# Kernel optimization log

Measured on AMD Instinct MI355X. Metric: run time of the kernel, lower is better.

Reference implementation:

```python
import jax, jax.numpy as jnp
import numpy as np

V, E, L, D, B, S = 50000, 512, 1024, 10, 1024, 50
N_NODES = L - 1  # internal Huffman nodes (balanced tree from uniform label counts)
LN_EPS = 1e-5
N_HIDDEN = 10


def _build_tree():
    # balanced binary tree in heap order: node at depth t for leaf l is (2^t - 1) + (l >> (D - t))
    l = np.arange(L)[:, None]
    t = np.arange(D)[None, :]
    bits = ((l >> (D - 1 - t)) & 1).astype(np.int32)          # [L, D] path direction bits
    paths = ((2 ** t - 1) + (l >> (D - t))).astype(np.int32)  # [L, D] internal node ids
    return paths, bits


def setup_inputs() -> dict:
    key = jax.random.key(0)
    k1, k2, k3, k4, k5, k6 = jax.random.split(key, 6)
    paths, bits = _build_tree()
    return {
        "input_ids": jax.random.randint(k1, (B, S), 0, V),
        "emb_table": jax.random.normal(k2, (V, E), dtype=jnp.float32) * 0.02,
        "W_h": jax.random.normal(k3, (E, E), dtype=jnp.float32) * (1.0 / np.sqrt(E)),
        "b_h": jax.random.normal(k4, (E,), dtype=jnp.float32) * 0.01,
        "theta_W": jax.random.normal(k5, (N_NODES, E, 2), dtype=jnp.float32) * (1.0 / np.sqrt(E)),
        "theta_b": jax.random.normal(k6, (N_NODES, 2), dtype=jnp.float32) * 0.01,
        "paths": jnp.asarray(paths),
        "bits": jnp.asarray(bits),
    }


def reference(input_ids, emb_table, W_h, b_h, theta_W, theta_b, paths, bits):
    # embedding + mean pool over sequence
    x = jnp.take(emb_table, input_ids, axis=0).mean(axis=1)  # [B, E]
    # LayerNorm with default (non-learned) affine, created fresh in torch forward
    mu = x.mean(axis=-1, keepdims=True)
    var = x.var(axis=-1, keepdims=True)
    x = (x - mu) * jax.lax.rsqrt(var + LN_EPS)
    # repeated hidden linear (same weights, hidden_num times)
    for _ in range(N_HIDDEN):
        x = x @ W_h + b_h
    # hierarchical softmax: batched 2-way logits at every internal node
    logits = jnp.einsum('be,ned->bnd', x, theta_W) + theta_b  # [B, N, 2]
    probs = jax.nn.softmax(logits, axis=-1)                   # [B, N, 2]
    # gather each class's path probs and multiply along the path
    p = probs[:, paths, bits]                                  # [B, L, D]
    return jnp.prod(p, axis=-1)                                # [B, L]
```

## Files before the change

### kernel.cpp

```cpp
#include <hip/hip_runtime.h>
#include <math.h>

#define B_  1024
#define S_  50
#define E_  512
#define L_  1024
#define D_  10
#define NN  1023
#define LN_EPS 1e-5f
#define CBLK 72

typedef short short8 __attribute__((ext_vector_type(8)));
typedef float f32x4  __attribute__((ext_vector_type(4)));

union PackU { unsigned int u[4]; short8 s; };

__device__ inline void split8(const float r[8], short8& hi, short8& lo) {
    PackU H, L;
#pragma unroll
    for (int q = 0; q < 4; ++q) {
        const unsigned int u0 = __float_as_uint(r[2*q+0]);
        const unsigned int u1 = __float_as_uint(r[2*q+1]);
        H.u[q] = (u0 >> 16) | (u1 & 0xFFFF0000u);
        const float h0 = __uint_as_float(u0 & 0xFFFF0000u);
        const float h1 = __uint_as_float(u1 & 0xFFFF0000u);
        const float l0 = r[2*q+0] - h0;
        const float l1 = r[2*q+1] - h1;
        unsigned int p;
        asm("v_cvt_pk_bf16_f32 %0, %1, %2" : "=v"(p) : "v"(l0), "v"(l1));
        L.u[q] = p;
    }
    hi = H.s; lo = L.s;
}

struct FragBuf { float4 a[2][2]; float4 b[2][2]; };

__device__ inline void loadbuf(FragBuf& f,
                               const float* pa0, const float* pa1,
                               const float* pb0, const float* pb1, int off) {
    f.a[0][0] = *reinterpret_cast<const float4*>(pa0 + off);
    f.a[0][1] = *reinterpret_cast<const float4*>(pa0 + off + 4);
    f.a[1][0] = *reinterpret_cast<const float4*>(pa1 + off);
    f.a[1][1] = *reinterpret_cast<const float4*>(pa1 + off + 4);
    f.b[0][0] = *reinterpret_cast<const float4*>(pb0 + off);
    f.b[0][1] = *reinterpret_cast<const float4*>(pb0 + off + 4);
    f.b[1][0] = *reinterpret_cast<const float4*>(pb1 + off);
    f.b[1][1] = *reinterpret_cast<const float4*>(pb1 + off + 4);
}

template<int TERMS>
__device__ inline void compbuf(const FragBuf& f, f32x4 acc[2][2]) {
    short8 ah[2], al[2], bh[2], bl[2];
#pragma unroll
    for (int i = 0; i < 2; ++i) {
        const float ra[8] = {f.a[i][0].x, f.a[i][0].y, f.a[i][0].z, f.a[i][0].w,
                             f.a[i][1].x, f.a[i][1].y, f.a[i][1].z, f.a[i][1].w};
        split8(ra, ah[i], al[i]);
        const float rb[8] = {f.b[i][0].x, f.b[i][0].y, f.b[i][0].z, f.b[i][0].w,
                             f.b[i][1].x, f.b[i][1].y, f.b[i][1].z, f.b[i][1].w};
        split8(rb, bh[i], bl[i]);
    }
#pragma unroll
    for (int i = 0; i < 2; ++i)
#pragma unroll
        for (int j = 0; j < 2; ++j) {
            acc[i][j] = __builtin_amdgcn_mfma_f32_16x16x32_bf16(ah[i], bh[j], acc[i][j], 0, 0, 0);
            acc[i][j] = __builtin_amdgcn_mfma_f32_16x16x32_bf16(ah[i], bl[j], acc[i][j], 0, 0, 0);
            acc[i][j] = __builtin_amdgcn_mfma_f32_16x16x32_bf16(al[i], bh[j], acc[i][j], 0, 0, 0);
            if (TERMS == 4)
                acc[i][j] = __builtin_amdgcn_mfma_f32_16x16x32_bf16(al[i], bl[j], acc[i][j], 0, 0, 0);
        }
}

template<int TERMS>
__device__ inline void gemm_k512(const float* pa0, const float* pa1,
                                 const float* pb0, const float* pb1,
                                 f32x4 acc[2][2]) {
    FragBuf f0, f1;
    loadbuf(f0, pa0, pa1, pb0, pb1, 0);
#pragma unroll 1
    for (int kt = 0; kt < 16; kt += 2) {
        loadbuf(f1, pa0, pa1, pb0, pb1, (kt + 1) * 32);
        compbuf<TERMS>(f0, acc);
        if (kt + 2 < 16) loadbuf(f0, pa0, pa1, pb0, pb1, (kt + 2) * 32);
        compbuf<TERMS>(f1, acc);
    }
}

__device__ inline void do_embed_row(const int* __restrict__ ids,
                                    const float* __restrict__ emb,
                                    float* __restrict__ x, int b) {
    const int t = threadIdx.x;
    float a0 = 0.f, a1 = 0.f;
    const int* idr = ids + b * S_;
#pragma unroll 5
    for (int s = 0; s < S_; ++s) {
        const float2 v = *reinterpret_cast<const float2*>(emb + (long)idr[s] * E_ + 2 * t);
        a0 += v.x;
        a1 += v.y;
    }
    a0 *= (1.f / S_);
    a1 *= (1.f / S_);

    __shared__ float red[256];
    red[t] = a0 + a1;
    __syncthreads();
    for (int off = 128; off > 0; off >>= 1) {
        if (t < off) red[t] += red[t + off];
        __syncthreads();
    }
    const float mean = red[0] * (1.f / E_);
    __syncthreads();
    const float d0 = a0 - mean, d1 = a1 - mean;
    red[t] = d0 * d0 + d1 * d1;
    __syncthreads();
    for (int off = 128; off > 0; off >>= 1) {
        if (t < off) red[t] += red[t + off];
        __syncthreads();
    }
    const float var = red[0] * (1.f / E_);
    const float inv = 1.f / sqrtf(var + LN_EPS);
    float2 o; o.x = d0 * inv; o.y = d1 * inv;
    *reinterpret_cast<float2*>(x + b * E_ + 2 * t) = o;
}

__device__ inline void do_dpack(const float* __restrict__ thW,
                                float* __restrict__ Dm, int part) {
    const int total = NN * 256;
    const int nth = 64 * 256;
    for (int p = part * 256 + (int)threadIdx.x; p < total; p += nth) {
        const int n = p >> 8;
        const int kp = p & 255;
        const float4 v = *reinterpret_cast<const float4*>(thW + (long)n * 1024 + kp * 4);
        float2 d; d.x = v.y - v.x; d.y = v.w - v.z;
        *reinterpret_cast<float2*>(Dm + (long)n * E_ + kp * 2) = d;
    }
}

__device__ inline void do_compose0(const float* __restrict__ Wh, const float* __restrict__ bh,
                                   float* __restrict__ Q0, float* __restrict__ T0, int bid) {
    const int tid  = threadIdx.x;
    const int wid  = tid >> 6;
    const int lane = tid & 63;
    const int r_lo = lane & 15;
    const int kg   = lane >> 4;
    const int row_base = (bid >> 3) * 64 + (wid >> 1) * 32;
    const int col_base = (bid & 7) * 64 + (wid & 1) * 32;
    f32x4 acc[2][2] = {};
#pragma unroll 2
    for (int kt = 0; kt < E_; kt += 32) {
        const int ks = kt + kg * 8;
        short8 ah[2], al[2], bhf[2], blf[2];
#pragma unroll
        for (int i = 0; i < 2; ++i) {
            const int row = row_base + i * 16 + r_lo;
            const float* ap = (row < E_) ? (Wh + (long)row * E_ + ks) : (bh + ks);
            const float4 v0 = *reinterpret_cast<const float4*>(ap);
            const float4 v1 = *reinterpret_cast<const float4*>(ap + 4);
            const float rr[8] = {v0.x, v0.y, v0.z, v0.w, v1.x, v1.y, v1.z, v1.w};
            split8(rr, ah[i], al[i]);
        }
#pragma unroll
        for (int j = 0; j < 2; ++j) {
            const int c = col_base + j * 16 + r_lo;
            float rr[8];
#pragma unroll
            for (int q = 0; q < 8; ++q) rr[q] = Wh[(long)(ks + q) * E_ + c];
            split8(rr, bhf[j], blf[j]);
        }
#pragma unroll
        for (int i = 0; i < 2; ++i)
#pragma unroll
            for (int j = 0; j < 2; ++j) {
                acc[i][j] = __builtin_amdgcn_mfma_f32_16x16x32_bf16(ah[i], bhf[j], acc[i][j], 0, 0, 0);
                acc[i][j] = __builtin_amdgcn_mfma_f32_16x16x32_bf16(ah[i], blf[j], acc[i][j], 0, 0, 0);
                acc[i][j] = __builtin_amdgcn_mfma_f32_16x16x32_bf16(al[i], bhf[j], acc[i][j], 0, 0, 0);
                acc[i][j] = __builtin_amdgcn_mfma_f32_16x16x32_bf16(al[i], blf[j], acc[i][j], 0, 0, 0);
            }
    }
#pragma unroll
    for (int j = 0; j < 2; ++j) {
        const int col = col_base + j * 16 + r_lo;
        const float bb = bh[col];
#pragma unroll
        for (int i = 0; i < 2; ++i) {
            const int row0 = row_base + i * 16 + kg * 4;
            float4 tv;
#pragma unroll
            for (int r2 = 0; r2 < 4; ++r2) {
                const int row = row0 + r2;
                float v = acc[i][j][r2];
                if (row == E_) v += bb;
                if (row <= E_) Q0[(long)row * E_ + col] = v;
                ((float*)&tv)[r2] = v;
            }
            if (row0 + 3 < E_) {
                *reinterpret_cast<float4*>(T0 + (long)col * E_ + row0) = tv;
            }
        }
    }
}

__device__ inline void do_compose(const float* __restrict__ A,
                                  const float* __restrict__ Bt,
                                  const float* __restrict__ Bbias,
                                  float* __restrict__ C, float* __restrict__ Ct,
                                  int bid) {
    const int tid  = threadIdx.x;
    const int wid  = tid >> 6;
    const int lane = tid & 63;
    const int r_lo = lane & 15;
    const int kg   = lane >> 4;
    const int row_base = (bid >> 3) * 64 + (wid >> 1) * 32;
    const int col_base = (bid & 7) * 64 + (wid & 1) * 32;

    int ra0 = row_base + r_lo;        if (ra0 > E_) ra0 = E_;
    int ra1 = row_base + 16 + r_lo;   if (ra1 > E_) ra1 = E_;
    const float* pa0 = A + (long)ra0 * E_ + kg * 8;
    const float* pa1 = A + (long)ra1 * E_ + kg * 8;
    const float* pb0 = Bt + (long)(col_base + r_lo) * E_ + kg * 8;
    const float* pb1 = Bt + (long)(col_base + 16 + r_lo) * E_ + kg * 8;

    f32x4 acc[2][2] = {};
    gemm_k512<4>(pa0, pa1, pb0, pb1, acc);

#pragma unroll
    for (int j = 0; j < 2; ++j) {
        const int col = col_base + j * 16 + r_lo;
        const float bb = Bbias[col];
#pragma unroll
        for (int i = 0; i < 2; ++i) {
            const int row0 = row_base + i * 16 + kg * 4;
            float4 tv;
#pragma unroll
            for (int r2 = 0; r2 < 4; ++r2) {
                const int row = row0 + r2;
                float v = acc[i][j][r2];
                if (row == E_) v += bb;
                if (row <= E_) C[(long)row * E_ + col] = v;
                ((float*)&tv)[r2] = v;
            }
            if (row0 + 3 < E_) {
                *reinterpret_cast<float4*>(Ct + (long)col * E_ + row0) = tv;
            }
        }
    }
}

__device__ inline void do_apply(const float* __restrict__ X,
                                const float* __restrict__ Mt,
                                const float* __restrict__ bias,
                                float* __restrict__ Y,
                                int tr, int tc) {
    const int tid  = threadIdx.x;
    const int wid  = tid >> 6;
    const int lane = tid & 63;
    const int r_lo = lane & 15;
    const int kg   = lane >> 4;
    const int row_base = tr * 64 + (wid >> 1) * 32;
    const int col_base = tc * 64 + (wid & 1) * 32;

    const float* pa0 = X + (long)(row_base + r_lo) * E_ + kg * 8;
    const float* pa1 = X + (long)(row_base + 16 + r_lo) * E_ + kg * 8;
    const float* pb0 = Mt + (long)(col_base + r_lo) * E_ + kg * 8;
    const float* pb1 = Mt + (long)(col_base + 16 + r_lo) * E_ + kg * 8;

    f32x4 acc[2][2] = {};
    gemm_k512<3>(pa0, pa1, pb0, pb1, acc);

#pragma unroll
    for (int j = 0; j < 2; ++j) {
        const int col = col_base + j * 16 + r_lo;
        const float bb = bias[col];
#pragma unroll
        for (int i = 0; i < 2; ++i) {
#pragma unroll
            for (int r2 = 0; r2 < 4; ++r2) {
                const int row = row_base + i * 16 + kg * 4 + r2;
                Y[(long)row * E_ + col] = acc[i][j][r2] + bb;
            }
        }
    }
}

__global__ __launch_bounds__(256) void k_fused0(const float* __restrict__ Wh,
                                                const float* __restrict__ bh,
                                                float* __restrict__ Q0, float* __restrict__ T0,
                                                const int* __restrict__ ids,
                                                const float* __restrict__ emb,
                                                float* __restrict__ xa,
                                                const float* __restrict__ thW,
                                                float* __restrict__ Dm) {
    const int bid = blockIdx.x;
    if (bid < CBLK)            do_compose0(Wh, bh, Q0, T0, bid);
    else if (bid < CBLK + 512) do_embed_row(ids, emb, xa, bid - CBLK);
    else                       do_dpack(thW, Dm, bid - CBLK - 512);
}

__global__ __launch_bounds__(256) void k_fused1(const float* __restrict__ Q0,
                                                const float* __restrict__ T0,
                                                float* __restrict__ Q1, float* __restrict__ T1,
                                                const int* __restrict__ ids,
                                                const float* __restrict__ emb,
                                                float* __restrict__ xa) {
    const int bid = blockIdx.x;
    if (bid < CBLK) do_compose(Q0, T0, Q0 + (long)E_ * E_, Q1, T1, bid);
    else            do_embed_row(ids, emb, xa, 512 + (bid - CBLK));
}

__global__ __launch_bounds__(256) void k_fused2(const float* __restrict__ Q1,
                                                const float* __restrict__ T1,
                                                float* __restrict__ Q2, float* __restrict__ T2,
                                                const float* __restrict__ xa,
                                                const float* __restrict__ T0,
                                                const float* __restrict__ Q0,
                                                float* __restrict__ y1) {
    const int bid = blockIdx.x;
    if (bid < CBLK) {
        do_compose(Q1, T1, Q1 + (long)E_ * E_, Q2, T2, bid);
    } else {
        const int t = bid - CBLK;
        do_apply(xa, T0, Q0 + (long)E_ * E_, y1, t >> 3, t & 7);
    }
}

__global__ __launch_bounds__(256) void k_apply8(const float* __restrict__ y1,
                                                const float* __restrict__ T2,
                                                const float* __restrict__ Q2,
                                                float* __restrict__ y2) {
    do_apply(y1, T2, Q2 + (long)E_ * E_, y2, blockIdx.x >> 3, blockIdx.x & 7);
}

__global__ __launch_bounds__(256) void k_theta(const float* __restrict__ X,
                                               const float* __restrict__ Dm,
                                               const float* __restrict__ thb,
                                               float* __restrict__ Sm) {
    const int tid  = threadIdx.x;
    const int wid  = tid >> 6;
    const int lane = tid & 63;
    const int r_lo = lane & 15;
    const int kg   = lane >> 4;
    const int tr = blockIdx.x >> 4;
    const int tc = blockIdx.x & 15;
    const int row_base = tr * 64 + (wid >> 1) * 32;
    const int col_base = tc * 64 + (wid & 1) * 32;

    int c0 = col_base + r_lo;        if (c0 > NN - 1) c0 = NN - 1;
    int c1 = col_base + 16 + r_lo;   if (c1 > NN - 1) c1 = NN - 1;
    const float* pa0 = X + (long)(row_base + r_lo) * E_ + kg * 8;
    const float* pa1 = X + (long)(row_base + 16 + r_lo) * E_ + kg * 8;
    const float* pb0 = Dm + (long)c0 * E_ + kg * 8;
    const float* pb1 = Dm + (long)c1 * E_ + kg * 8;

    f32x4 acc[2][2] = {};
    gemm_k512<3>(pa0, pa1, pb0, pb1, acc);

#pragma unroll
    for (int j = 0; j < 2; ++j) {
        const int col = col_base + j * 16 + r_lo;
        const int cc = (col > NN - 1) ? (NN - 1) : col;
        const float bb = thb[2 * cc + 1] - thb[2 * cc + 0];
#pragma unroll
        for (int i = 0; i < 2; ++i) {
#pragma unroll
            for (int r2 = 0; r2 < 4; ++r2) {
                const int row = row_base + i * 16 + kg * 4 + r2;
                if (col < NN) {
                    Sm[(long)row * NN + col] = acc[i][j][r2] + bb;
                }
            }
        }
    }
}

__global__ __launch_bounds__(256) void k_leaf_tree(const float* __restrict__ Sm,
                                                   float* __restrict__ out) {
    __shared__ float buf[2][L_];
    const int b = blockIdx.x;
    const int tid = threadIdx.x;
    const float* srow = Sm + b * NN;
    if (tid == 0) buf[0][0] = 1.f;
    __syncthreads();
    int cur = 0;
    for (int t = 0; t < D_; ++t) {
        const int cnt = 1 << t;
        const int base = cnt - 1;
        for (int j = tid; j < cnt; j += 256) {
            const float z = srow[base + j];
            const float s = 1.f / (1.f + __expf(-z));
            const float a = buf[cur][j];
            buf[cur ^ 1][2*j + 1] = a * s;
            buf[cur ^ 1][2*j + 0] = a - a * s;
        }
        __syncthreads();
        cur ^= 1;
    }
    reinterpret_cast<float4*>(out + b * L_)[tid] =
        reinterpret_cast<const float4*>(buf[cur])[tid];
}

extern "C" void kernel_launch(void* const* d_in, const int* in_sizes, int n_in,
                              void* d_out, int out_size, void* d_ws, size_t ws_size,
                              hipStream_t stream) {
    const int*   ids = (const int*)d_in[0];
    const float* emb = (const float*)d_in[1];
    const float* Wh  = (const float*)d_in[2];
    const float* bh  = (const float*)d_in[3];
    const float* thW = (const float*)d_in[4];
    const float* thb = (const float*)d_in[5];
    float* out = (float*)d_out;

    char* ws = (char*)d_ws;
    float* xa = (float*)(ws);
    float* y1 = (float*)(ws + (2u << 20));
    float* y2 = (float*)(ws + (4u << 20));
    float* sm = (float*)(ws + (6u << 20));
    float* Dm = (float*)(ws + (11u << 20));
    const size_t QS = 0x140000;
    float* Q0 = (float*)(ws + (14u << 20));
    float* Q1 = (float*)(ws + (14u << 20) + QS);
    float* Q2 = (float*)(ws + (14u << 20) + 2 * QS);
    float* T0 = (float*)(ws + (20u << 20));
    float* T1 = (float*)(ws + (21u << 20));
    float* T2 = (float*)(ws + (22u << 20));

    k_fused0<<<CBLK + 512 + 64, 256, 0, stream>>>(Wh, bh, Q0, T0, ids, emb, xa, thW, Dm);

    k_fused1<<<CBLK + 512, 256, 0, stream>>>(Q0, T0, Q1, T1, ids, emb, xa);

    k_fused2<<<CBLK + 128, 256, 0, stream>>>(Q1, T1, Q2, T2, xa, T0, Q0, y1);

    k_apply8<<<128, 256, 0, stream>>>(y1, T2, Q2, y2);

    k_theta<<<256, 256, 0, stream>>>(y2, Dm, thb, sm);

    k_leaf_tree<<<B_, 256, 0, stream>>>(sm, out);
}
```

Measured before the change: 105.5 us.

## Store intermediates as pre-split bf16 hi/lo pairs instead of fp32

Measured after the change: 105.2 us. Within noise of the previous version (-0.4%).

```diff
diff --git a/kernel.cpp b/kernel.cpp
--- a/kernel.cpp
+++ b/kernel.cpp
@@ -1,4 +1,5 @@
 #include <hip/hip_runtime.h>
+#include <hip/hip_bf16.h>
 #include <math.h>
 
 #define B_  1024
@@ -12,6 +13,8 @@
 
 typedef short short8 __attribute__((ext_vector_type(8)));
 typedef float f32x4  __attribute__((ext_vector_type(4)));
+typedef unsigned short u16;
+typedef unsigned int   u32;
 
 union PackU { unsigned int u[4]; short8 s; };
 
@@ -33,63 +36,78 @@
     hi = H.s; lo = L.s;
 }
 
-struct FragBuf { float4 a[2][2]; float4 b[2][2]; };
-
-__device__ inline void loadbuf(FragBuf& f,
-                               const float* pa0, const float* pa1,
-                               const float* pb0, const float* pb1, int off) {
-    f.a[0][0] = *reinterpret_cast<const float4*>(pa0 + off);
-    f.a[0][1] = *reinterpret_cast<const float4*>(pa0 + off + 4);
-    f.a[1][0] = *reinterpret_cast<const float4*>(pa1 + off);
-    f.a[1][1] = *reinterpret_cast<const float4*>(pa1 + off + 4);
-    f.b[0][0] = *reinterpret_cast<const float4*>(pb0 + off);
-    f.b[0][1] = *reinterpret_cast<const float4*>(pb0 + off + 4);
-    f.b[1][0] = *reinterpret_cast<const float4*>(pb1 + off);
-    f.b[1][1] = *reinterpret_cast<const float4*>(pb1 + off + 4);
+__device__ inline void split1(float v, u16& h, u16& l) {
+    const unsigned int u = __float_as_uint(v);
+    h = (u16)(u >> 16);
+    const float hf = __uint_as_float(u & 0xFFFF0000u);
+    const float lo = v - hf;
+    unsigned int p;
+    asm("v_cvt_pk_bf16_f32 %0, %1, %2" : "=v"(p) : "v"(lo), "v"(lo));
+    l = (u16)(p & 0xFFFFu);
+}
+
+__device__ inline void split2(float v0, float v1, u32& hw, u32& lw) {
+    const unsigned int u0 = __float_as_uint(v0);
+    const unsigned int u1 = __float_as_uint(v1);
+    hw = (u0 >> 16) | (u1 & 0xFFFF0000u);
+    const float h0 = __uint_as_float(u0 & 0xFFFF0000u);
+    const float h1 = __uint_as_float(u1 & 0xFFFF0000u);
+    const float l0 = v0 - h0;
+    const float l1 = v1 - h1;
+    asm("v_cvt_pk_bf16_f32 %0, %1, %2" : "=v"(lw) : "v"(l0), "v"(l1));
+}
+
+struct BFrag { short8 ah[2], al[2], bh[2], bl[2]; };
+
+__device__ inline void loadB(BFrag& f,
+                             const u16* pah0, const u16* pal0,
+                             const u16* pah1, const u16* pal1,
+                             const u16* pbh0, const u16* pbl0,
+                             const u16* pbh1, const u16* pbl1, int off) {
+    f.ah[0] = *reinterpret_cast<const short8*>(pah0 + off);
+    f.al[0] = *reinterpret_cast<const short8*>(pal0 + off);
+    f.ah[1] = *reinterpret_cast<const short8*>(pah1 + off);
+    f.al[1] = *reinterpret_cast<const short8*>(pal1 + off);
+    f.bh[0] = *reinterpret_cast<const short8*>(pbh0 + off);
+    f.bl[0] = *reinterpret_cast<const short8*>(pbl0 + off);
+    f.bh[1] = *reinterpret_cast<const short8*>(pbh1 + off);
+    f.bl[1] = *reinterpret_cast<const short8*>(pbl1 + off);
 }
 
 template<int TERMS>
-__device__ inline void compbuf(const FragBuf& f, f32x4 acc[2][2]) {
-    short8 ah[2], al[2], bh[2], bl[2];
-#pragma unroll
-    for (int i = 0; i < 2; ++i) {
-        const float ra[8] = {f.a[i][0].x, f.a[i][0].y, f.a[i][0].z, f.a[i][0].w,
-                             f.a[i][1].x, f.a[i][1].y, f.a[i][1].z, f.a[i][1].w};
-        split8(ra, ah[i], al[i]);
-        const float rb[8] = {f.b[i][0].x, f.b[i][0].y, f.b[i][0].z, f.b[i][0].w,
-                             f.b[i][1].x, f.b[i][1].y, f.b[i][1].z, f.b[i][1].w};
-        split8(rb, bh[i], bl[i]);
-    }
+__device__ inline void compB(const BFrag& f, f32x4 acc[2][2]) {
 #pragma unroll
     for (int i = 0; i < 2; ++i)
 #pragma unroll
         for (int j = 0; j < 2; ++j) {
-            acc[i][j] = __builtin_amdgcn_mfma_f32_16x16x32_bf16(ah[i], bh[j], acc[i][j], 0, 0, 0);
-            acc[i][j] = __builtin_amdgcn_mfma_f32_16x16x32_bf16(ah[i], bl[j], acc[i][j], 0, 0, 0);
-            acc[i][j] = __builtin_amdgcn_mfma_f32_16x16x32_bf16(al[i], bh[j], acc[i][j], 0, 0, 0);
+            acc[i][j] = __builtin_amdgcn_mfma_f32_16x16x32_bf16(f.ah[i], f.bh[j], acc[i][j], 0, 0, 0);
+            acc[i][j] = __builtin_amdgcn_mfma_f32_16x16x32_bf16(f.ah[i], f.bl[j], acc[i][j], 0, 0, 0);
+            acc[i][j] = __builtin_amdgcn_mfma_f32_16x16x32_bf16(f.al[i], f.bh[j], acc[i][j], 0, 0, 0);
             if (TERMS == 4)
-                acc[i][j] = __builtin_amdgcn_mfma_f32_16x16x32_bf16(al[i], bl[j], acc[i][j], 0, 0, 0);
+                acc[i][j] = __builtin_amdgcn_mfma_f32_16x16x32_bf16(f.al[i], f.bl[j], acc[i][j], 0, 0, 0);
         }
 }
 
 template<int TERMS>
-__device__ inline void gemm_k512(const float* pa0, const float* pa1,
-                                 const float* pb0, const float* pb1,
-                                 f32x4 acc[2][2]) {
-    FragBuf f0, f1;
-    loadbuf(f0, pa0, pa1, pb0, pb1, 0);
+__device__ inline void gemmB(const u16* pah0, const u16* pal0,
+                             const u16* pah1, const u16* pal1,
+                             const u16* pbh0, const u16* pbl0,
+                             const u16* pbh1, const u16* pbl1,
+                             f32x4 acc[2][2]) {
+    BFrag f0, f1;
+    loadB(f0, pah0, pal0, pah1, pal1, pbh0, pbl0, pbh1, pbl1, 0);
 #pragma unroll 1
     for (int kt = 0; kt < 16; kt += 2) {
-        loadbuf(f1, pa0, pa1, pb0, pb1, (kt + 1) * 32);
-        compbuf<TERMS>(f0, acc);
-        if (kt + 2 < 16) loadbuf(f0, pa0, pa1, pb0, pb1, (kt + 2) * 32);
-        compbuf<TERMS>(f1, acc);
+        loadB(f1, pah0, pal0, pah1, pal1, pbh0, pbl0, pbh1, pbl1, (kt + 1) * 32);
+        compB<TERMS>(f0, acc);
+        if (kt + 2 < 16) loadB(f0, pah0, pal0, pah1, pal1, pbh0, pbl0, pbh1, pbl1, (kt + 2) * 32);
+        compB<TERMS>(f1, acc);
     }
 }
 
 __device__ inline void do_embed_row(const int* __restrict__ ids,
                                     const float* __restrict__ emb,
-                                    float* __restrict__ x, int b) {
+                                    u16* __restrict__ xah, u16* __restrict__ xal, int b) {
     const int t = threadIdx.x;
     float a0 = 0.f, a1 = 0.f;
     const int* idr = ids + b * S_;
@@ -120,25 +138,66 @@
     }
     const float var = red[0] * (1.f / E_);
     const float inv = 1.f / sqrtf(var + LN_EPS);
-    float2 o; o.x = d0 * inv; o.y = d1 * inv;
-    *reinterpret_cast<float2*>(x + b * E_ + 2 * t) = o;
+    u32 hw, lw;
+    split2(d0 * inv, d1 * inv, hw, lw);
+    *reinterpret_cast<u32*>(xah + (long)b * E_ + 2 * t) = hw;
+    *reinterpret_cast<u32*>(xal + (long)b * E_ + 2 * t) = lw;
 }
 
 __device__ inline void do_dpack(const float* __restrict__ thW,
-                                float* __restrict__ Dm, int part) {
+                                u16* __restrict__ Dh, u16* __restrict__ Dl, int part) {
     const int total = NN * 256;
     const int nth = 64 * 256;
     for (int p = part * 256 + (int)threadIdx.x; p < total; p += nth) {
         const int n = p >> 8;
         const int kp = p & 255;
         const float4 v = *reinterpret_cast<const float4*>(thW + (long)n * 1024 + kp * 4);
-        float2 d; d.x = v.y - v.x; d.y = v.w - v.z;
-        *reinterpret_cast<float2*>(Dm + (long)n * E_ + kp * 2) = d;
+        u32 hw, lw;
+        split2(v.y - v.x, v.w - v.z, hw, lw);
+        *reinterpret_cast<u32*>(Dh + (long)n * E_ + kp * 2) = hw;
+        *reinterpret_cast<u32*>(Dl + (long)n * E_ + kp * 2) = lw;
+    }
+}
+
+__device__ inline void compose_epilogue(f32x4 acc[2][2], int row_base, int col_base,
+                                        int kg, int r_lo,
+                                        const float* __restrict__ Bbias,
+                                        u16* __restrict__ Ch, u16* __restrict__ Cl,
+                                        u16* __restrict__ Th, u16* __restrict__ Tl,
+                                        float* __restrict__ cvec) {
+#pragma unroll
+    for (int j = 0; j < 2; ++j) {
+        const int col = col_base + j * 16 + r_lo;
+        const float bb = Bbias[col];
+#pragma unroll
+        for (int i = 0; i < 2; ++i) {
+            const int row0 = row_base + i * 16 + kg * 4;
+            union { ushort4 v; u16 e[4]; } th, tl;
+#pragma unroll
+            for (int r2 = 0; r2 < 4; ++r2) {
+                const int row = row0 + r2;
+                float v = acc[i][j][r2];
+                if (row == E_) { v += bb; cvec[col] = v; }
+                u16 h, l;
+                split1(v, h, l);
+                if (row <= E_ && Ch != nullptr) {
+                    Ch[(long)row * E_ + col] = h;
+                    Cl[(long)row * E_ + col] = l;
+                }
+                th.e[r2] = h; tl.e[r2] = l;
+            }
+            if (row0 + 3 < E_) {
+                *reinterpret_cast<ushort4*>(Th + (long)col * E_ + row0) = th.v;
+                *reinterpret_cast<ushort4*>(Tl + (long)col * E_ + row0) = tl.v;
+            }
+        }
     }
 }
 
 __device__ inline void do_compose0(const float* __restrict__ Wh, const float* __restrict__ bh,
-                                   float* __restrict__ Q0, float* __restrict__ T0, int bid) {
+                                   u16* __restrict__ Ch, u16* __restrict__ Cl,
+                                   u16* __restrict__ Th, u16* __restrict__ Tl,
+                                   float* __restrict__ cvec, int bid) {
     const int tid  = threadIdx.x;
     const int wid  = tid >> 6;
     const int lane = tid & 63;
@@ -178,34 +237,15 @@
                 acc[i][j] = __builtin_amdgcn_mfma_f32_16x16x32_bf16(al[i], blf[j], acc[i][j], 0, 0, 0);
             }
     }
-#pragma unroll
-    for (int j = 0; j < 2; ++j) {
-        const int col = col_base + j * 16 + r_lo;
-        const float bb = bh[col];
-#pragma unroll
-        for (int i = 0; i < 2; ++i) {
-            const int row0 = row_base + i * 16 + kg * 4;
-            float4 tv;
-#pragma unroll
-            for (int r2 = 0; r2 < 4; ++r2) {
-                const int row = row0 + r2;
-                float v = acc[i][j][r2];
-                if (row == E_) v += bb;
-                if (row <= E_) Q0[(long)row * E_ + col] = v;
-                ((float*)&tv)[r2] = v;
-            }
-            if (row0 + 3 < E_) {
-                *reinterpret_cast<float4*>(T0 + (long)col * E_ + row0) = tv;
-            }
-        }
-    }
-}
-
-__device__ inline void do_compose(const float* __restrict__ A,
-                                  const float* __restrict__ Bt,
-                                  const float* __restrict__ Bbias,
-                                  float* __restrict__ C, float* __restrict__ Ct,
-                                  int bid) {
+    compose_epilogue(acc, row_base, col_base, kg, r_lo, bh, Ch, Cl, Th, Tl, cvec);
+}
+
+__device__ inline void do_composeB(const u16* __restrict__ Ah, const u16* __restrict__ Al,
+                                   const u16* __restrict__ Bh, const u16* __restrict__ Bl,
+                                   const float* __restrict__ Bbias,
+                                   u16* __restrict__ Ch, u16* __restrict__ Cl,
+                                   u16* __restrict__ Th, u16* __restrict__ Tl,
+                                   float* __restrict__ cvec, int bid) {
     const int tid  = threadIdx.x;
     const int wid  = tid >> 6;
     const int lane = tid & 63;
@@ -216,42 +256,23 @@
 
     int ra0 = row_base + r_lo;        if (ra0 > E_) ra0 = E_;
     int ra1 = row_base + 16 + r_lo;   if (ra1 > E_) ra1 = E_;
-    const float* pa0 = A + (long)ra0 * E_ + kg * 8;
-    const float* pa1 = A + (long)ra1 * E_ + kg * 8;
-    const float* pb0 = Bt + (long)(col_base + r_lo) * E_ + kg * 8;
-    const float* pb1 = Bt + (long)(col_base + 16 + r_lo) * E_ + kg * 8;
+    const long rb0 = col_base + r_lo;
+    const long rb1 = col_base + 16 + r_lo;
 
     f32x4 acc[2][2] = {};
-    gemm_k512<4>(pa0, pa1, pb0, pb1, acc);
-
-#pragma unroll
-    for (int j = 0; j < 2; ++j) {
-        const int col = col_base + j * 16 + r_lo;
-        const float bb = Bbias[col];
-#pragma unroll
-        for (int i = 0; i < 2; ++i) {
-            const int row0 = row_base + i * 16 + kg * 4;
-            float4 tv;
-#pragma unroll
-            for (int r2 = 0; r2 < 4; ++r2) {
-                const int row = row0 + r2;
-                float v = acc[i][j][r2];
-                if (row == E_) v += bb;
-                if (row <= E_) C[(long)row * E_ + col] = v;
-                ((float*)&tv)[r2] = v;
-            }
-            if (row0 + 3 < E_) {
-                *reinterpret_cast<float4*>(Ct + (long)col * E_ + row0) = tv;
-            }
-        }
-    }
-}
-
-__device__ inline void do_apply(const float* __restrict__ X,
-                                const float* __restrict__ Mt,
-                                const float* __restrict__ bias,
-                                float* __restrict__ Y,
-                                int tr, int tc) {
+    gemmB<4>(Ah + (long)ra0 * E_ + kg * 8, Al + (long)ra0 * E_ + kg * 8,
+             Ah + (long)ra1 * E_ + kg * 8, Al + (long)ra1 * E_ + kg * 8,
+             Bh + rb0 * E_ + kg * 8,       Bl + rb0 * E_ + kg * 8,
+             Bh + rb1 * E_ + kg * 8,       Bl + rb1 * E_ + kg * 8, acc);
+
+    compose_epilogue(acc, row_base, col_base, kg, r_lo, Bbias, Ch, Cl, Th, Tl, cvec);
+}
+
+__device__ inline void do_applyB(const u16* __restrict__ Xh, const u16* __restrict__ Xl,
+                                 const u16* __restrict__ Mh, const u16* __restrict__ Ml,
+                                 const float* __restrict__ cvec,
+                                 u16* __restrict__ Yh, u16* __restrict__ Yl,
+                                 int tr, int tc) {
     const int tid  = threadIdx.x;
     const int wid  = tid >> 6;
     const int lane = tid & 63;
@@ -260,24 +281,30 @@
     const int row_base = tr * 64 + (wid >> 1) * 32;
     const int col_base = tc * 64 + (wid & 1) * 32;
 
-    const float* pa0 = X + (long)(row_base + r_lo) * E_ + kg * 8;
-    const float* pa1 = X + (long)(row_base + 16 + r_lo) * E_ + kg * 8;
-    const float* pb0 = Mt + (long)(col_base + r_lo) * E_ + kg * 8;
-    const float* pb1 = Mt + (long)(col_base + 16 + r_lo) * E_ + kg * 8;
+    const long ra0 = row_base + r_lo;
+    const long ra1 = row_base + 16 + r_lo;
+    const long rb0 = col_base + r_lo;
+    const long rb1 = col_base + 16 + r_lo;
 
     f32x4 acc[2][2] = {};
-    gemm_k512<3>(pa0, pa1, pb0, pb1, acc);
+    gemmB<3>(Xh + ra0 * E_ + kg * 8, Xl + ra0 * E_ + kg * 8,
+             Xh + ra1 * E_ + kg * 8, Xl + ra1 * E_ + kg * 8,
+             Mh + rb0 * E_ + kg * 8, Ml + rb0 * E_ + kg * 8,
+             Mh + rb1 * E_ + kg * 8, Ml + rb1 * E_ + kg * 8, acc);
 
 #pragma unroll
     for (int j = 0; j < 2; ++j) {
         const int col = col_base + j * 16 + r_lo;
-        const float bb = bias[col];
+        const float bb = cvec[col];
 #pragma unroll
         for (int i = 0; i < 2; ++i) {
 #pragma unroll
             for (int r2 = 0; r2 < 4; ++r2) {
                 const int row = row_base + i * 16 + kg * 4 + r2;
-                Y[(long)row * E_ + col] = acc[i][j][r2] + bb;
+                u16 h, l;
+                split1(acc[i][j][r2] + bb, h, l);
+                Yh[(long)row * E_ + col] = h;
+                Yl[(long)row * E_ + col] = l;
             }
         }
     }
@@ -285,54 +312,61 @@
 
 __global__ __launch_bounds__(256) void k_fused0(const float* __restrict__ Wh,
                                                 const float* __restrict__ bh,
-                                                float* __restrict__ Q0, float* __restrict__ T0,
+                                                u16* __restrict__ Ch0, u16* __restrict__ Cl0,
+                                                u16* __restrict__ Th0, u16* __restrict__ Tl0,
+                                                float* __restrict__ cvec0,
                                                 const int* __restrict__ ids,
                                                 const float* __restrict__ emb,
-                                                float* __restrict__ xa,
+                                                u16* __restrict__ xah, u16* __restrict__ xal,
                                                 const float* __restrict__ thW,
-                                                float* __restrict__ Dm) {
+                                                u16* __restrict__ Dh, u16* __restrict__ Dl) {
     const int bid = blockIdx.x;
-    if (bid < CBLK)            do_compose0(Wh, bh, Q0, T0, bid);
-    else if (bid < CBLK + 512) do_embed_row(ids, emb, xa, bid - CBLK);
-    else                       do_dpack(thW, Dm, bid - CBLK - 512);
-}
-
-__global__ __launch_bounds__(256) void k_fused1(const float* __restrict__ Q0,
-                                                const float* __restrict__ T0,
-                                                float* __restrict__ Q1, float* __restrict__ T1,
+    if (bid < CBLK)            do_compose0(Wh, bh, Ch0, Cl0, Th0, Tl0, cvec0, bid);
+    else if (bid < CBLK + 512) do_embed_row(ids, emb, xah, xal, bid - CBLK);
+    else                       do_dpack(thW, Dh, Dl, bid - CBLK - 512);
+}
+
+__global__ __launch_bounds__(256) void k_fused1(const u16* __restrict__ Ch0, const u16* __restrict__ Cl0,
+                                                const u16* __restrict__ Th0, const u16* __restrict__ Tl0,
+                                                const float* __restrict__ cvec0,
+                                                u16* __restrict__ Ch1, u16* __restrict__ Cl1,
+                                                u16* __restrict__ Th1, u16* __restrict__ Tl1,
+                                                float* __restrict__ cvec1,
                                                 const int* __restrict__ ids,
                                                 const float* __restrict__ emb,
-                                                float* __restrict__ xa) {
+                                                u16* __restrict__ xah, u16* __restrict__ xal) {
     const int bid = blockIdx.x;
-    if (bid < CBLK) do_compose(Q0, T0, Q0 + (long)E_ * E_, Q1, T1, bid);
-    else            do_embed_row(ids, emb, xa, 512 + (bid - CBLK));
-}
-
-__global__ __launch_bounds__(256) void k_fused2(const float* __restrict__ Q1,
-                                                const float* __restrict__ T1,
-                                                float* __restrict__ Q2, float* __restrict__ T2,
-                                                const float* __restrict__ xa,
-                                                const float* __restrict__ T0,
-                                                const float* __restrict__ Q0,
-                                                float* __restrict__ y1) {
+    if (bid < CBLK) do_composeB(Ch0, Cl0, Th0, Tl0, cvec0, Ch1, Cl1, Th1, Tl1, cvec1, bid);
+    else            do_embed_row(ids, emb, xah, xal, 512 + (bid - CBLK));
+}
+
+__global__ __launch_bounds__(256) void k_fused2(const u16* __restrict__ Ch1, const u16* __restrict__ Cl1,
+                                                const u16* __restrict__ Th1, const u16* __restrict__ Tl1,
+                                                const float* __restrict__ cvec1,
+                                                u16* __restrict__ Th2, u16* __restrict__ Tl2,
+                                                float* __restrict__ cvec2,
+                                                const u16* __restrict__ xah, const u16* __restrict__ xal,
+                                                const u16* __restrict__ Th0, const u16* __restrict__ Tl0,
+                                                const float* __restrict__ cvec0,
+                                                u16* __restrict__ y1h, u16* __restrict__ y1l) {
     const int bid = blockIdx.x;
     if (bid < CBLK) {
-        do_compose(Q1, T1, Q1 + (long)E_ * E_, Q2, T2, bid);
+        do_composeB(Ch1, Cl1, Th1, Tl1, cvec1, nullptr, nullptr, Th2, Tl2, cvec2, bid);
     } else {
         const int t = bid - CBLK;
-        do_apply(xa, T0, Q0 + (long)E_ * E_, y1, t >> 3, t & 7);
-    }
-}
-
-__global__ __launch_bounds__(256) void k_apply8(const float* __restrict__ y1,
-                                                const float* __restrict__ T2,
-                                                const float* __restrict__ Q2,
-                                                float* __restrict__ y2) {
-    do_apply(y1, T2, Q2 + (long)E_ * E_, y2, blockIdx.x >> 3, blockIdx.x & 7);
-}
-
-__global__ __launch_bounds__(256) void k_theta(const float* __restrict__ X,
-                                               const float* __restrict__ Dm,
+        do_applyB(xah, xal, Th0, Tl0, cvec0, y1h, y1l, t >> 3, t & 7);
+    }
+}
+
+__global__ __launch_bounds__(256) void k_apply8(const u16* __restrict__ y1h, const u16* __restrict__ y1l,
+                                                const u16* __restrict__ Th2, const u16* __restrict__ Tl2,
+                                                const float* __restrict__ cvec2,
+                                                u16* __restrict__ y2h, u16* __restrict__ y2l) {
+    do_applyB(y1h, y1l, Th2, Tl2, cvec2, y2h, y2l, blockIdx.x >> 3, blockIdx.x & 7);
+}
+
+__global__ __launch_bounds__(256) void k_theta(const u16* __restrict__ Xh, const u16* __restrict__ Xl,
+                                               const u16* __restrict__ Dh, const u16* __restrict__ Dl,
                                                const float* __restrict__ thb,
                                                float* __restrict__ Sm) {
     const int tid  = threadIdx.x;
@@ -345,15 +379,16 @@
     const int row_base = tr * 64 + (wid >> 1) * 32;
     const int col_base = tc * 64 + (wid & 1) * 32;
 
-    int c0 = col_base + r_lo;        if (c0 > NN - 1) c0 = NN - 1;
-    int c1 = col_base + 16 + r_lo;   if (c1 > NN - 1) c1 = NN - 1;
-    const float* pa0 = X + (long)(row_base + r_lo) * E_ + kg * 8;
-    const float* pa1 = X + (long)(row_base + 16 + r_lo) * E_ + kg * 8;
-    const float* pb0 = Dm + (long)c0 * E_ + kg * 8;
-    const float* pb1 = Dm + (long)c1 * E_ + kg * 8;
+    long c0 = col_base + r_lo;        if (c0 > NN - 1) c0 = NN - 1;
+    long c1 = col_base + 16 + r_lo;   if (c1 > NN - 1) c1 = NN - 1;
+    const long ra0 = row_base + r_lo;
+    const long ra1 = row_base + 16 + r_lo;
 
     f32x4 acc[2][2] = {};
-    gemm_k512<3>(pa0, pa1, pb0, pb1, acc);
+    gemmB<3>(Xh + ra0 * E_ + kg * 8, Xl + ra0 * E_ + kg * 8,
+             Xh + ra1 * E_ + kg * 8, Xl + ra1 * E_ + kg * 8,
+             Dh + c0 * E_ + kg * 8,  Dl + c0 * E_ + kg * 8,
+             Dh + c1 * E_ + kg * 8,  Dl + c1 * E_ + kg * 8, acc);
 
 #pragma unroll
     for (int j = 0; j < 2; ++j) {
@@ -378,7 +413,7 @@
     __shared__ float buf[2][L_];
     const int b = blockIdx.x;
     const int tid = threadIdx.x;
-    const float* srow = Sm + b * NN;
+    const float* srow = Sm + (long)b * NN;
     if (tid == 0) buf[0][0] = 1.f;
     __syncthreads();
     int cur = 0;
@@ -395,7 +430,7 @@
         __syncthreads();
         cur ^= 1;
     }
-    reinterpret_cast<float4*>(out + b * L_)[tid] =
+    reinterpret_cast<float4*>(out + (long)b * L_)[tid] =
         reinterpret_cast<const float4*>(buf[cur])[tid];
 }
 
@@ -411,28 +446,44 @@
     float* out = (float*)d_out;
 
     char* ws = (char*)d_ws;
-    float* xa = (float*)(ws);
-    float* y1 = (float*)(ws + (2u << 20));
-    float* y2 = (float*)(ws + (4u << 20));
-    float* sm = (float*)(ws + (6u << 20));
-    float* Dm = (float*)(ws + (11u << 20));
-    const size_t QS = 0x140000;
-    float* Q0 = (float*)(ws + (14u << 20));
-    float* Q1 = (float*)(ws + (14u << 20) + QS);
-    float* Q2 = (float*)(ws + (14u << 20) + 2 * QS);
-    float* T0 = (float*)(ws + (20u << 20));
-    float* T1 = (float*)(ws + (21u << 20));
-    float* T2 = (float*)(ws + (22u << 20));
-
-    k_fused0<<<CBLK + 512 + 64, 256, 0, stream>>>(Wh, bh, Q0, T0, ids, emb, xa, thW, Dm);
-
-    k_fused1<<<CBLK + 512, 256, 0, stream>>>(Q0, T0, Q1, T1, ids, emb, xa);
-
-    k_fused2<<<CBLK + 128, 256, 0, stream>>>(Q1, T1, Q2, T2, xa, T0, Q0, y1);
-
-    k_apply8<<<128, 256, 0, stream>>>(y1, T2, Q2, y2);
-
-    k_theta<<<256, 256, 0, stream>>>(y2, Dm, thb, sm);
+    const size_t MB = 1u << 20;
+    u16* xah = (u16*)(ws + 0 * MB);
+    u16* xal = (u16*)(ws + 1 * MB);
+    u16* y1h = (u16*)(ws + 2 * MB);
+    u16* y1l = (u16*)(ws + 3 * MB);
+    u16* y2h = (u16*)(ws + 4 * MB);
+    u16* y2l = (u16*)(ws + 5 * MB);
+    float* sm = (float*)(ws + 6 * MB);
+    u16* Dh  = (u16*)(ws + 11 * MB);
+    u16* Dl  = (u16*)(ws + 12 * MB);
+    u16* Ch0 = (u16*)(ws + 13 * MB);
+    u16* Cl0 = (u16*)(ws + 14 * MB);
+    u16* Ch1 = (u16*)(ws + 15 * MB);
+    u16* Cl1 = (u16*)(ws + 16 * MB);
+    u16* Th0 = (u16*)(ws + 17 * MB);
+    u16* Tl0 = (u16*)(ws + 17 * MB + 512 * 1024);
+    u16* Th1 = (u16*)(ws + 18 * MB);
+    u16* Tl1 = (u16*)(ws + 18 * MB + 512 * 1024);
+    u16* Th2 = (u16*)(ws + 19 * MB);
+    u16* Tl2 = (u16*)(ws + 19 * MB + 512 * 1024);
+    float* cvec0 = (float*)(ws + 20 * MB);
+    float* cvec1 = (float*)(ws + 20 * MB + 4096);
+    float* cvec2 = (float*)(ws + 20 * MB + 8192);
+
+    k_fused0<<<CBLK + 512 + 64, 256, 0, stream>>>(Wh, bh, Ch0, Cl0, Th0, Tl0, cvec0,
+                                                  ids, emb, xah, xal, thW, Dh, Dl);
+
+    k_fused1<<<CBLK + 512, 256, 0, stream>>>(Ch0, Cl0, Th0, Tl0, cvec0,
+                                             Ch1, Cl1, Th1, Tl1, cvec1,
+                                             ids, emb, xah, xal);
+
+    k_fused2<<<CBLK + 128, 256, 0, stream>>>(Ch1, Cl1, Th1, Tl1, cvec1,
+                                             Th2, Tl2, cvec2,
+                                             xah, xal, Th0, Tl0, cvec0, y1h, y1l);
+
+    k_apply8<<<128, 256, 0, stream>>>(y1h, y1l, Th2, Tl2, cvec2, y2h, y2l);
+
+    k_theta<<<256, 256, 0, stream>>>(y2h, y2l, Dh, Dl, thb, sm);
 
     k_leaf_tree<<<B_, 256, 0, stream>>>(sm, out);
 }
```
